# Optimization experiments

Hardware: AMD Instinct MI355X
Metric: run time of the kernel (lower is better)

Reference implementation:

```python
import jax, jax.numpy as jnp
import numpy as np

B, L, D1, D2, N = 4, 2048, 1024, 1024, 4096

def setup_inputs() -> dict:
    key = jax.random.key(0)
    k1, k2, k3 = jax.random.split(key, 3)
    inputs = jax.random.normal(k1, (B, L, D1), dtype=jnp.float32)
    key_param_tokens = jax.random.normal(k2, (N, D1), dtype=jnp.float32) * 0.02
    value_param_tokens = jax.random.normal(k3, (N, D2), dtype=jnp.float32) * 0.02
    return {"inputs": inputs, "key_param_tokens": key_param_tokens, "value_param_tokens": value_param_tokens}

def reference(inputs, key_param_tokens, value_param_tokens):
    # scores: [B, L, N] = query @ key^T (scale_factor = 1, no mask, dropout_p = 0)
    attn_weight = jnp.einsum('bld,nd->bln', inputs, key_param_tokens)
    n = attn_weight.shape[-1]
    # 'l2_norm_gelu': L2-normalize over the param-token axis, rescale by sqrt(n), then exact GELU
    l2 = jnp.sqrt(jnp.sum(attn_weight * attn_weight, axis=-1, keepdims=True))
    normed = attn_weight / l2 * jnp.sqrt(jnp.asarray(n, attn_weight.dtype))
    attn_weight = jax.nn.gelu(normed, approximate=False)
    # output: [B, L, D2]
    return jnp.einsum('bln,nd->bld', attn_weight, value_param_tokens)
```

## Files before the change

kernel.cpp:

```cpp
#include <hip/hip_runtime.h>
#include <hip/hip_bf16.h>
#include <math.h>
#include <stdint.h>

typedef __attribute__((ext_vector_type(8))) short short8;
typedef __attribute__((ext_vector_type(4))) float f32x4;

__device__ inline short f2bf(float x) {
  union { float f; uint32_t u; } c; c.f = x;
  uint32_t r = (c.u + 0x7FFFu + ((c.u >> 16) & 1u)) >> 16;
  return (short)(uint16_t)r;
}
__device__ inline float bf2f(short s) {
  union { uint32_t u; float f; } c; c.u = ((uint32_t)(uint16_t)s) << 16;
  return c.f;
}

__device__ inline void gload16(const short* src, const char* ldsdst) {
  __builtin_amdgcn_global_load_lds(
      (const __attribute__((address_space(1))) void*)src,
      (__attribute__((address_space(3))) void*)ldsdst, 16, 0, 0);
}

#define BAR __builtin_amdgcn_s_barrier()
#define VMC(n) asm volatile("s_waitcnt vmcnt(" #n ")" ::: "memory")

__global__ void f32_to_bf16_kernel(const float* __restrict__ in,
                                   short* __restrict__ out, int n8) {
  int i = blockIdx.x * blockDim.x + threadIdx.x;
  if (i >= n8) return;
  const float4* p = (const float4*)(in + (size_t)i * 8);
  float4 a = p[0], b = p[1];
  short8 o;
  o[0] = f2bf(a.x); o[1] = f2bf(a.y); o[2] = f2bf(a.z); o[3] = f2bf(a.w);
  o[4] = f2bf(b.x); o[5] = f2bf(b.y); o[6] = f2bf(b.z); o[7] = f2bf(b.w);
  *(short8*)(out + (size_t)i * 8) = o;
}

__global__ void transpose_bf16_kernel(const float* __restrict__ V,
                                      short* __restrict__ Vt,
                                      int rows, int cols) {
  __shared__ float tile[64][65];
  int n0 = blockIdx.x * 64;
  int d0 = blockIdx.y * 64;
  int t = threadIdx.x;
#pragma unroll
  for (int r = 0; r < 16; ++r) {
    int idx = t + 256 * r;
    int rr = idx >> 6, cc = idx & 63;
    tile[rr][cc] = V[(size_t)(n0 + rr) * cols + d0 + cc];
  }
  __syncthreads();
#pragma unroll
  for (int r = 0; r < 16; ++r) {
    int idx = t + 256 * r;
    int dd = idx >> 6, nn = idx & 63;
    Vt[(size_t)(d0 + dd) * rows + n0 + nn] = f2bf(tile[nn][dd]);
  }
}

__global__ __launch_bounds__(512, 2) void gemm1_kernel(
    const short* __restrict__ A, const short* __restrict__ B,
    short* __restrict__ S, float* __restrict__ rowss) {
  constexpr int K = 1024, N = 4096, NT = K / 64;
  __shared__ char lds[2 * 65536];
  const int t = threadIdx.x, lane = t & 63, w = t >> 6;
  const int wm = w >> 2, wn = w & 3;
  const int idx = lane & 15, g = lane >> 4;
  const int bid = blockIdx.x;
  const int id2 = (bid & 7) * 64 + (bid >> 3);
  const int row0 = (id2 >> 4) * 256, col0 = (id2 & 15) * 256;

  const int srow = t >> 3;
  const int ksl = (t & 7) ^ (srow & 7);
  const short* gA = A + (size_t)(row0 + srow) * K + ksl * 8;
  const short* gB = B + (size_t)(col0 + srow) * K + ksl * 8;

  auto stageA = [&](int buf, int frow, int kt) {
#pragma unroll
    for (int r = 0; r < 2; ++r)
      gload16(gA + (size_t)(frow + r * 64) * K + kt,
              &lds[buf * 65536 + (frow + r * 64) * 128 + t * 16]);
  };
  auto stageB = [&](int buf, int frow, int kt) {
#pragma unroll
    for (int r = 0; r < 2; ++r)
      gload16(gB + (size_t)(frow + r * 64) * K + kt,
              &lds[buf * 65536 + 32768 + (frow + r * 64) * 128 + t * 16]);
  };

  const int xv = (idx & 7) << 4;
  short8 a[4][2], b[2][2][2];
  auto lda = [&](int buf, int mh) {
#pragma unroll
    for (int f = 0; f < 4; ++f)
#pragma unroll
      for (int ks = 0; ks < 2; ++ks) {
        int row = mh * 128 + wm * 64 + f * 16 + idx;
        int byte = row * 128 + ((ks * 64 + g * 16) ^ xv);
        a[f][ks] = *(const short8*)&lds[buf * 65536 + byte];
      }
  };
  auto ldb = [&](int buf, int nh) {
#pragma unroll
    for (int nf = 0; nf < 2; ++nf)
#pragma unroll
      for (int ks = 0; ks < 2; ++ks) {
        int col = nh * 128 + wn * 32 + nf * 16 + idx;
        int byte = col * 128 + ((ks * 64 + g * 16) ^ xv);
        b[nh][nf][ks] = *(const short8*)&lds[buf * 65536 + 32768 + byte];
      }
  };

  f32x4 acc[8][4] = {};
  auto MF = [&](int mh, int nh) {
    __builtin_amdgcn_s_setprio(1);
#pragma unroll
    for (int ks = 0; ks < 2; ++ks)
#pragma unroll
      for (int f = 0; f < 4; ++f)
#pragma unroll
        for (int n = 0; n < 2; ++n)
          acc[mh * 4 + f][nh * 2 + n] = __builtin_amdgcn_mfma_f32_16x16x32_bf16(
              a[f][ks], b[nh][n][ks], acc[mh * 4 + f][nh * 2 + n], 0, 0, 0);
    __builtin_amdgcn_s_setprio(0);
  };

  stageA(0, 0, 0);
  stageB(0, 0, 0);
  stageB(0, 128, 0);
  stageA(0, 128, 0);
  VMC(2);
  BAR;

  for (int tb = 0; tb < NT; tb += 2) {
#pragma unroll
    for (int u = 0; u < 2; ++u) {
      const int T = tb + u, buf = u, nbuf = u ^ 1;
      const int kt1 = (T + 1) * 64;
      const bool more = (T + 1 < NT);
      lda(buf, 0); ldb(buf, 0);
      if (more) stageA(nbuf, 0, kt1);
      MF(0, 0);
      ldb(buf, 1);
      if (more) stageB(nbuf, 0, kt1);
      MF(0, 1);
      if (more) { VMC(4); } else { VMC(0); }
      BAR;
      lda(buf, 1);
      if (more) stageB(nbuf, 128, kt1);
      MF(1, 1);
      if (more) stageA(nbuf, 128, kt1);
      MF(1, 0);
      if (more) {
        VMC(2);
        BAR;
      }
    }
  }

#pragma unroll
  for (int mf = 0; mf < 8; ++mf) {
#pragma unroll
    for (int j = 0; j < 4; ++j) {
      const int row = row0 + wm * 64 + (mf & 3) * 16 + (mf >> 2) * 128 + g * 4 + j;
      float ss = 0.f;
#pragma unroll
      for (int nf = 0; nf < 4; ++nf) {
        const float v = acc[mf][nf][j];
        ss += v * v;
        const int col = col0 + wn * 32 + (nf & 1) * 16 + (nf >> 1) * 128 + idx;
        S[(size_t)row * N + col] = f2bf(v);
      }
      ss += __shfl_xor(ss, 1);
      ss += __shfl_xor(ss, 2);
      ss += __shfl_xor(ss, 4);
      ss += __shfl_xor(ss, 8);
      if (idx == 0) atomicAdd(&rowss[row], ss);
    }
  }
}

__global__ __launch_bounds__(512, 2) void gemm2_kernel(
    const short* __restrict__ A, const short* __restrict__ B,
    float* __restrict__ C) {
  constexpr int K = 4096, N = 1024, NT = K / 64;
  __shared__ char lds[2 * 49152];
  const int t = threadIdx.x, lane = t & 63, w = t >> 6;
  const int wm = w >> 1, wn = w & 1;
  const int idx = lane & 15, g = lane >> 4;
  const int bid = blockIdx.x;
  const int id2 = (bid & 7) * 32 + (bid >> 3);
  const int row0 = (id2 >> 3) * 256, col0 = (id2 & 7) * 128;

  const int srow = t >> 3;
  const int ksl = (t & 7) ^ (srow & 7);
  const short* gA = A + (size_t)(row0 + srow) * K + ksl * 8;
  const short* gB = B + (size_t)(col0 + srow) * K + ksl * 8;

  auto stageAr = [&](int buf, int fr, int kt) {
    gload16(gA + (size_t)(fr)*K + kt, &lds[buf * 49152 + fr * 128 + t * 16]);
  };
  auto stageB = [&](int buf, int kt) {
#pragma unroll
    for (int r = 0; r < 2; ++r)
      gload16(gB + (size_t)(r * 64) * K + kt,
              &lds[buf * 49152 + 32768 + r * 8192 + t * 16]);
  };

  const int xv = (idx & 7) << 4;
  short8 a[2][2], b[4][2];
  auto lda = [&](int buf, int mh) {
#pragma unroll
    for (int f = 0; f < 2; ++f)
#pragma unroll
      for (int ks = 0; ks < 2; ++ks) {
        int row = mh * 128 + wm * 32 + f * 16 + idx;
        int byte = row * 128 + ((ks * 64 + g * 16) ^ xv);
        a[f][ks] = *(const short8*)&lds[buf * 49152 + byte];
      }
  };
  auto ldb = [&](int buf) {
#pragma unroll
    for (int nf = 0; nf < 4; ++nf)
#pragma unroll
      for (int ks = 0; ks < 2; ++ks) {
        int col = wn * 64 + nf * 16 + idx;
        int byte = col * 128 + ((ks * 64 + g * 16) ^ xv);
        b[nf][ks] = *(const short8*)&lds[buf * 49152 + 32768 + byte];
      }
  };

  f32x4 acc[4][4] = {};
  auto MF = [&](int mh) {
    __builtin_amdgcn_s_setprio(1);
#pragma unroll
    for (int ks = 0; ks < 2; ++ks)
#pragma unroll
      for (int f = 0; f < 2; ++f)
#pragma unroll
        for (int nf = 0; nf < 4; ++nf)
          acc[mh * 2 + f][nf] = __builtin_amdgcn_mfma_f32_16x16x32_bf16(
              a[f][ks], b[nf][ks], acc[mh * 2 + f][nf], 0, 0, 0);
    __builtin_amdgcn_s_setprio(0);
  };

  stageB(0, 0);
  stageAr(0, 0, 0);
  stageAr(0, 64, 0);
  stageAr(0, 128, 0);
  stageAr(0, 192, 0);
  VMC(2);
  BAR;

  for (int tb = 0; tb < NT; tb += 2) {
#pragma unroll
    for (int u = 0; u < 2; ++u) {
      const int T = tb + u, buf = u, nbuf = u ^ 1;
      const int kt1 = (T + 1) * 64;
      const bool more = (T + 1 < NT);
      ldb(buf); lda(buf, 0);
      if (more) { stageB(nbuf, kt1); stageAr(nbuf, 0, kt1); stageAr(nbuf, 64, kt1); }
      MF(0);
      if (more) { VMC(4); } else { VMC(0); }
      BAR;
      lda(buf, 1);
      if (more) { stageAr(nbuf, 128, kt1); stageAr(nbuf, 192, kt1); }
      MF(1);
      if (more) {
        VMC(2);
        BAR;
      }
    }
  }

#pragma unroll
  for (int mf = 0; mf < 4; ++mf)
#pragma unroll
    for (int j = 0; j < 4; ++j) {
      const int row = row0 + wm * 32 + (mf & 1) * 16 + (mf >> 1) * 128 + g * 4 + j;
#pragma unroll
      for (int nf = 0; nf < 4; ++nf)
        C[(size_t)row * N + col0 + wn * 64 + nf * 16 + idx] = acc[mf][nf][j];
    }
}

__global__ void norm_gelu_kernel(short* __restrict__ S,
                                 const float* __restrict__ rowss, int total8) {
  int i = blockIdx.x * blockDim.x + threadIdx.x;
  if (i >= total8) return;
  size_t base = (size_t)i * 8;
  int row = (int)(base >> 12);
  float scale = 64.0f * rsqrtf(rowss[row]);
  short8 v = *(short8*)(S + base);
  short8 o;
#pragma unroll
  for (int k = 0; k < 8; ++k) {
    float x = bf2f(v[k]) * scale;
    float gl = 0.5f * x * (1.0f + erff(x * 0.70710678118654752f));
    o[k] = f2bf(gl);
  }
  *(short8*)(S + base) = o;
}

extern "C" void kernel_launch(void* const* d_in, const int* in_sizes, int n_in,
                              void* d_out, int out_size, void* d_ws,
                              size_t ws_size, hipStream_t stream) {
  const float* X = (const float*)d_in[0];
  const float* Kp = (const float*)d_in[1];
  const float* Vp = (const float*)d_in[2];
  float* out = (float*)d_out;

  const int M = 8192, D1 = 1024, Nn = 4096, D2 = 1024;

  char* ws = (char*)d_ws;
  short* Xb = (short*)ws; ws += (size_t)M * D1 * 2;
  short* Kb = (short*)ws; ws += (size_t)Nn * D1 * 2;
  short* Vt = (short*)ws; ws += (size_t)D2 * Nn * 2;
  short* S  = (short*)ws; ws += (size_t)M * Nn * 2;
  float* rowss = (float*)ws;
  (void)ws_size;

  hipMemsetAsync(rowss, 0, M * sizeof(float), stream);
  f32_to_bf16_kernel<<<(M * D1 / 8 + 255) / 256, 256, 0, stream>>>(X, Xb, M * D1 / 8);
  f32_to_bf16_kernel<<<(Nn * D1 / 8 + 255) / 256, 256, 0, stream>>>(Kp, Kb, Nn * D1 / 8);
  transpose_bf16_kernel<<<dim3(Nn / 64, D2 / 64), 256, 0, stream>>>(Vp, Vt, Nn, D2);

  gemm1_kernel<<<512, 512, 0, stream>>>(Xb, Kb, S, rowss);
  norm_gelu_kernel<<<(M * Nn / 8 + 255) / 256, 256, 0, stream>>>(S, rowss, M * Nn / 8);
  gemm2_kernel<<<256, 512, 0, stream>>>(S, Vt, out);
}
```

Baseline: 194.4 us.

## Switch both GEMMs to 32x32x16 MFMA tiles and merge conversion kernels

Both GEMM kernels now use the 32x32x16 bf16 MFMA instruction instead of 16x16x32. Fragment loads, LDS swizzle offsets, accumulator layout and epilogue row/column mapping are rewritten to match, including an extra shuffle in the row sum-of-squares reduction. The larger MFMA tile means fewer instructions and fewer LDS fragment reads per FLOP, at the cost of a different register layout and wider per-lane accumulators. The two fp32-to-bf16 conversion launches are also fused into a single kernel to save a launch.

```diff
diff --git a/kernel.cpp b/kernel.cpp
--- a/kernel.cpp
+++ b/kernel.cpp
@@ -4,7 +4,7 @@
 #include <stdint.h>
 
 typedef __attribute__((ext_vector_type(8))) short short8;
-typedef __attribute__((ext_vector_type(4))) float f32x4;
+typedef __attribute__((ext_vector_type(16))) float f32x16;
 
 __device__ inline short f2bf(float x) {
   union { float f; uint32_t u; } c; c.f = x;
@@ -25,16 +25,19 @@
 #define BAR __builtin_amdgcn_s_barrier()
 #define VMC(n) asm volatile("s_waitcnt vmcnt(" #n ")" ::: "memory")
 
-__global__ void f32_to_bf16_kernel(const float* __restrict__ in,
-                                   short* __restrict__ out, int n8) {
+__global__ void cvt2_kernel(const float* __restrict__ X, const float* __restrict__ Kp,
+                            short* __restrict__ Xb, short* __restrict__ Kb,
+                            int n8x, int n8tot) {
   int i = blockIdx.x * blockDim.x + threadIdx.x;
-  if (i >= n8) return;
-  const float4* p = (const float4*)(in + (size_t)i * 8);
+  if (i >= n8tot) return;
+  const float* src = (i < n8x) ? X + (size_t)i * 8 : Kp + (size_t)(i - n8x) * 8;
+  short* dst = (i < n8x) ? Xb + (size_t)i * 8 : Kb + (size_t)(i - n8x) * 8;
+  const float4* p = (const float4*)src;
   float4 a = p[0], b = p[1];
   short8 o;
   o[0] = f2bf(a.x); o[1] = f2bf(a.y); o[2] = f2bf(a.z); o[3] = f2bf(a.w);
   o[4] = f2bf(b.x); o[5] = f2bf(b.y); o[6] = f2bf(b.z); o[7] = f2bf(b.w);
-  *(short8*)(out + (size_t)i * 8) = o;
+  *(short8*)dst = o;
 }
 
 __global__ void transpose_bf16_kernel(const float* __restrict__ V,
@@ -66,15 +69,14 @@
   __shared__ char lds[2 * 65536];
   const int t = threadIdx.x, lane = t & 63, w = t >> 6;
   const int wm = w >> 2, wn = w & 3;
-  const int idx = lane & 15, g = lane >> 4;
+  const int r32 = lane & 31, l5 = lane >> 5;
   const int bid = blockIdx.x;
   const int id2 = (bid & 7) * 64 + (bid >> 3);
   const int row0 = (id2 >> 4) * 256, col0 = (id2 & 15) * 256;
 
-  const int srow = t >> 3;
-  const int ksl = (t & 7) ^ (srow & 7);
-  const short* gA = A + (size_t)(row0 + srow) * K + ksl * 8;
-  const short* gB = B + (size_t)(col0 + srow) * K + ksl * 8;
+  const int sxor = ((t & 7) ^ ((t >> 3) & 7)) * 8;
+  const short* gA = A + (size_t)(row0 + (t >> 3)) * K + sxor;
+  const short* gB = B + (size_t)(col0 + (t >> 3)) * K + sxor;
 
   auto stageA = [&](int buf, int frow, int kt) {
 #pragma unroll
@@ -89,40 +91,37 @@
               &lds[buf * 65536 + 32768 + (frow + r * 64) * 128 + t * 16]);
   };
 
-  const int xv = (idx & 7) << 4;
-  short8 a[4][2], b[2][2][2];
+  int qb[4];
+#pragma unroll
+  for (int c = 0; c < 4; ++c) qb[c] = ((c * 2 + l5) ^ (r32 & 7)) << 4;
+
+  short8 a[2][4], b[2][4];
   auto lda = [&](int buf, int mh) {
 #pragma unroll
-    for (int f = 0; f < 4; ++f)
-#pragma unroll
-      for (int ks = 0; ks < 2; ++ks) {
-        int row = mh * 128 + wm * 64 + f * 16 + idx;
-        int byte = row * 128 + ((ks * 64 + g * 16) ^ xv);
-        a[f][ks] = *(const short8*)&lds[buf * 65536 + byte];
+    for (int fr = 0; fr < 2; ++fr)
+#pragma unroll
+      for (int c = 0; c < 4; ++c) {
+        const int row = mh * 128 + wm * 64 + fr * 32 + r32;
+        a[fr][c] = *(const short8*)&lds[buf * 65536 + row * 128 + qb[c]];
       }
   };
   auto ldb = [&](int buf, int nh) {
 #pragma unroll
-    for (int nf = 0; nf < 2; ++nf)
-#pragma unroll
-      for (int ks = 0; ks < 2; ++ks) {
-        int col = nh * 128 + wn * 32 + nf * 16 + idx;
-        int byte = col * 128 + ((ks * 64 + g * 16) ^ xv);
-        b[nh][nf][ks] = *(const short8*)&lds[buf * 65536 + 32768 + byte];
-      }
-  };
-
-  f32x4 acc[8][4] = {};
-  auto MF = [&](int mh, int nh) {
+    for (int c = 0; c < 4; ++c) {
+      const int col = wn * 64 + nh * 32 + r32;
+      b[nh][c] = *(const short8*)&lds[buf * 65536 + 32768 + col * 128 + qb[c]];
+    }
+  };
+
+  f32x16 acc[4][2] = {};
+  auto MFQ = [&](int mh, int nh) {
     __builtin_amdgcn_s_setprio(1);
 #pragma unroll
-    for (int ks = 0; ks < 2; ++ks)
-#pragma unroll
-      for (int f = 0; f < 4; ++f)
-#pragma unroll
-        for (int n = 0; n < 2; ++n)
-          acc[mh * 4 + f][nh * 2 + n] = __builtin_amdgcn_mfma_f32_16x16x32_bf16(
-              a[f][ks], b[nh][n][ks], acc[mh * 4 + f][nh * 2 + n], 0, 0, 0);
+    for (int c = 0; c < 4; ++c)
+#pragma unroll
+      for (int fr = 0; fr < 2; ++fr)
+        acc[mh * 2 + fr][nh] = __builtin_amdgcn_mfma_f32_32x32x16_bf16(
+            a[fr][c], b[nh][c], acc[mh * 2 + fr][nh], 0, 0, 0);
     __builtin_amdgcn_s_setprio(0);
   };
 
@@ -141,17 +140,17 @@
       const bool more = (T + 1 < NT);
       lda(buf, 0); ldb(buf, 0);
       if (more) stageA(nbuf, 0, kt1);
-      MF(0, 0);
+      MFQ(0, 0);
       ldb(buf, 1);
       if (more) stageB(nbuf, 0, kt1);
-      MF(0, 1);
+      MFQ(0, 1);
       if (more) { VMC(4); } else { VMC(0); }
       BAR;
       lda(buf, 1);
       if (more) stageB(nbuf, 128, kt1);
-      MF(1, 1);
+      MFQ(1, 1);
       if (more) stageA(nbuf, 128, kt1);
-      MF(1, 0);
+      MFQ(1, 0);
       if (more) {
         VMC(2);
         BAR;
@@ -160,23 +159,25 @@
   }
 
 #pragma unroll
-  for (int mf = 0; mf < 8; ++mf) {
-#pragma unroll
-    for (int j = 0; j < 4; ++j) {
-      const int row = row0 + wm * 64 + (mf & 3) * 16 + (mf >> 2) * 128 + g * 4 + j;
+  for (int mf = 0; mf < 4; ++mf) {
+    const int mh = mf >> 1, fr = mf & 1;
+#pragma unroll
+    for (int j = 0; j < 16; ++j) {
+      const int row = row0 + mh * 128 + wm * 64 + fr * 32 +
+                      (j & 3) + 8 * (j >> 2) + 4 * l5;
       float ss = 0.f;
 #pragma unroll
-      for (int nf = 0; nf < 4; ++nf) {
-        const float v = acc[mf][nf][j];
+      for (int nh = 0; nh < 2; ++nh) {
+        const float v = acc[mf][nh][j];
         ss += v * v;
-        const int col = col0 + wn * 32 + (nf & 1) * 16 + (nf >> 1) * 128 + idx;
-        S[(size_t)row * N + col] = f2bf(v);
+        S[(size_t)row * N + col0 + wn * 64 + nh * 32 + r32] = f2bf(v);
       }
       ss += __shfl_xor(ss, 1);
       ss += __shfl_xor(ss, 2);
       ss += __shfl_xor(ss, 4);
       ss += __shfl_xor(ss, 8);
-      if (idx == 0) atomicAdd(&rowss[row], ss);
+      ss += __shfl_xor(ss, 16);
+      if (r32 == 0) atomicAdd(&rowss[row], ss);
     }
   }
 }
@@ -188,15 +189,14 @@
   __shared__ char lds[2 * 49152];
   const int t = threadIdx.x, lane = t & 63, w = t >> 6;
   const int wm = w >> 1, wn = w & 1;
-  const int idx = lane & 15, g = lane >> 4;
+  const int r32 = lane & 31, l5 = lane >> 5;
   const int bid = blockIdx.x;
   const int id2 = (bid & 7) * 32 + (bid >> 3);
   const int row0 = (id2 >> 3) * 256, col0 = (id2 & 7) * 128;
 
-  const int srow = t >> 3;
-  const int ksl = (t & 7) ^ (srow & 7);
-  const short* gA = A + (size_t)(row0 + srow) * K + ksl * 8;
-  const short* gB = B + (size_t)(col0 + srow) * K + ksl * 8;
+  const int sxor = ((t & 7) ^ ((t >> 3) & 7)) * 8;
+  const short* gA = A + (size_t)(row0 + (t >> 3)) * K + sxor;
+  const short* gB = B + (size_t)(col0 + (t >> 3)) * K + sxor;
 
   auto stageAr = [&](int buf, int fr, int kt) {
     gload16(gA + (size_t)(fr)*K + kt, &lds[buf * 49152 + fr * 128 + t * 16]);
@@ -208,40 +208,37 @@
               &lds[buf * 49152 + 32768 + r * 8192 + t * 16]);
   };
 
-  const int xv = (idx & 7) << 4;
-  short8 a[2][2], b[4][2];
+  int qb[4];
+#pragma unroll
+  for (int c = 0; c < 4; ++c) qb[c] = ((c * 2 + l5) ^ (r32 & 7)) << 4;
+
+  short8 a[4], b[2][4];
   auto lda = [&](int buf, int mh) {
 #pragma unroll
-    for (int f = 0; f < 2; ++f)
-#pragma unroll
-      for (int ks = 0; ks < 2; ++ks) {
-        int row = mh * 128 + wm * 32 + f * 16 + idx;
-        int byte = row * 128 + ((ks * 64 + g * 16) ^ xv);
-        a[f][ks] = *(const short8*)&lds[buf * 49152 + byte];
-      }
+    for (int c = 0; c < 4; ++c) {
+      const int row = mh * 128 + wm * 32 + r32;
+      a[c] = *(const short8*)&lds[buf * 49152 + row * 128 + qb[c]];
+    }
   };
   auto ldb = [&](int buf) {
 #pragma unroll
-    for (int nf = 0; nf < 4; ++nf)
-#pragma unroll
-      for (int ks = 0; ks < 2; ++ks) {
-        int col = wn * 64 + nf * 16 + idx;
-        int byte = col * 128 + ((ks * 64 + g * 16) ^ xv);
-        b[nf][ks] = *(const short8*)&lds[buf * 49152 + 32768 + byte];
-      }
-  };
-
-  f32x4 acc[4][4] = {};
+    for (int nf = 0; nf < 2; ++nf)
+#pragma unroll
+      for (int c = 0; c < 4; ++c) {
+        const int col = wn * 64 + nf * 32 + r32;
+        b[nf][c] = *(const short8*)&lds[buf * 49152 + 32768 + col * 128 + qb[c]];
+      }
+  };
+
+  f32x16 acc[2][2] = {};
   auto MF = [&](int mh) {
     __builtin_amdgcn_s_setprio(1);
 #pragma unroll
-    for (int ks = 0; ks < 2; ++ks)
-#pragma unroll
-      for (int f = 0; f < 2; ++f)
-#pragma unroll
-        for (int nf = 0; nf < 4; ++nf)
-          acc[mh * 2 + f][nf] = __builtin_amdgcn_mfma_f32_16x16x32_bf16(
-              a[f][ks], b[nf][ks], acc[mh * 2 + f][nf], 0, 0, 0);
+    for (int c = 0; c < 4; ++c)
+#pragma unroll
+      for (int nf = 0; nf < 2; ++nf)
+        acc[mh][nf] = __builtin_amdgcn_mfma_f32_32x32x16_bf16(
+            a[c], b[nf][c], acc[mh][nf], 0, 0, 0);
     __builtin_amdgcn_s_setprio(0);
   };
 
@@ -275,13 +272,13 @@
   }
 
 #pragma unroll
-  for (int mf = 0; mf < 4; ++mf)
-#pragma unroll
-    for (int j = 0; j < 4; ++j) {
-      const int row = row0 + wm * 32 + (mf & 1) * 16 + (mf >> 1) * 128 + g * 4 + j;
-#pragma unroll
-      for (int nf = 0; nf < 4; ++nf)
-        C[(size_t)row * N + col0 + wn * 64 + nf * 16 + idx] = acc[mf][nf][j];
+  for (int mh = 0; mh < 2; ++mh)
+#pragma unroll
+    for (int j = 0; j < 16; ++j) {
+      const int row = row0 + mh * 128 + wm * 32 + (j & 3) + 8 * (j >> 2) + 4 * l5;
+#pragma unroll
+      for (int nf = 0; nf < 2; ++nf)
+        C[(size_t)row * N + col0 + wn * 64 + nf * 32 + r32] = acc[mh][nf][j];
     }
 }
 
@@ -322,8 +319,8 @@
   (void)ws_size;
 
   hipMemsetAsync(rowss, 0, M * sizeof(float), stream);
-  f32_to_bf16_kernel<<<(M * D1 / 8 + 255) / 256, 256, 0, stream>>>(X, Xb, M * D1 / 8);
-  f32_to_bf16_kernel<<<(Nn * D1 / 8 + 255) / 256, 256, 0, stream>>>(Kp, Kb, Nn * D1 / 8);
+  const int n8x = M * D1 / 8, n8k = Nn * D1 / 8;
+  cvt2_kernel<<<(n8x + n8k + 255) / 256, 256, 0, stream>>>(X, Kp, Xb, Kb, n8x, n8x + n8k);
   transpose_bf16_kernel<<<dim3(Nn / 64, D2 / 64), 256, 0, stream>>>(Vp, Vt, Nn, D2);
 
   gemm1_kernel<<<512, 512, 0, stream>>>(Xb, Kb, S, rowss);
```

New measurement: 264.0 us. 1.36x slower.

## Restructure gemm1 into quadrant schedule with deeper B prefetch and merged conversions

Applied to the files above, without the earlier changes.

Reorganizes the gemm1 warp tiling so each wave owns a contiguous 128-row by 64-column quadrant. The main loop is rescheduled into four quadrant MFMA phases with barriers and explicit lgkmcnt waits, and B tiles are prefetched two k-steps ahead while A tiles are prefetched one step ahead. The two f32-to-bf16 conversion launches are also merged into a single kernel to save a launch. The extra barriers per phase may add synchronization stalls that offset the gain from deeper prefetch.

```diff
diff --git a/kernel.cpp b/kernel.cpp
--- a/kernel.cpp
+++ b/kernel.cpp
@@ -24,17 +24,25 @@
 
 #define BAR __builtin_amdgcn_s_barrier()
 #define VMC(n) asm volatile("s_waitcnt vmcnt(" #n ")" ::: "memory")
-
-__global__ void f32_to_bf16_kernel(const float* __restrict__ in,
-                                   short* __restrict__ out, int n8) {
+#define LGKM0                                          \
+  do {                                                 \
+    asm volatile("s_waitcnt lgkmcnt(0)" ::: "memory"); \
+    __builtin_amdgcn_sched_barrier(0);                 \
+  } while (0)
+
+__global__ void cvt2_kernel(const float* __restrict__ X, const float* __restrict__ Kp,
+                            short* __restrict__ Xb, short* __restrict__ Kb,
+                            int n8x, int n8tot) {
   int i = blockIdx.x * blockDim.x + threadIdx.x;
-  if (i >= n8) return;
-  const float4* p = (const float4*)(in + (size_t)i * 8);
+  if (i >= n8tot) return;
+  const float* src = (i < n8x) ? X + (size_t)i * 8 : Kp + (size_t)(i - n8x) * 8;
+  short* dst = (i < n8x) ? Xb + (size_t)i * 8 : Kb + (size_t)(i - n8x) * 8;
+  const float4* p = (const float4*)src;
   float4 a = p[0], b = p[1];
   short8 o;
   o[0] = f2bf(a.x); o[1] = f2bf(a.y); o[2] = f2bf(a.z); o[3] = f2bf(a.w);
   o[4] = f2bf(b.x); o[5] = f2bf(b.y); o[6] = f2bf(b.z); o[7] = f2bf(b.w);
-  *(short8*)(out + (size_t)i * 8) = o;
+  *(short8*)dst = o;
 }
 
 __global__ void transpose_bf16_kernel(const float* __restrict__ V,
@@ -71,90 +79,90 @@
   const int id2 = (bid & 7) * 64 + (bid >> 3);
   const int row0 = (id2 >> 4) * 256, col0 = (id2 & 15) * 256;
 
-  const int srow = t >> 3;
-  const int ksl = (t & 7) ^ (srow & 7);
-  const short* gA = A + (size_t)(row0 + srow) * K + ksl * 8;
-  const short* gB = B + (size_t)(col0 + srow) * K + ksl * 8;
-
-  auto stageA = [&](int buf, int frow, int kt) {
+  const int sxor = ((t & 7) ^ ((t >> 3) & 7)) * 8;
+  const short* gA = A + (size_t)(row0 + (t >> 3)) * K + sxor;
+  const short* gB = B + (size_t)(col0 + (t >> 3)) * K + sxor;
+
+  auto STGA = [&](int buf, int h, int T) {
 #pragma unroll
     for (int r = 0; r < 2; ++r)
-      gload16(gA + (size_t)(frow + r * 64) * K + kt,
-              &lds[buf * 65536 + (frow + r * 64) * 128 + t * 16]);
-  };
-  auto stageB = [&](int buf, int frow, int kt) {
+      gload16(gA + (size_t)(h * 128 + r * 64) * K + T * 64,
+              &lds[buf * 65536 + h * 16384 + r * 8192 + t * 16]);
+  };
+  auto STGB = [&](int buf, int h, int T) {
 #pragma unroll
     for (int r = 0; r < 2; ++r)
-      gload16(gB + (size_t)(frow + r * 64) * K + kt,
-              &lds[buf * 65536 + 32768 + (frow + r * 64) * 128 + t * 16]);
+      gload16(gB + (size_t)(h * 128 + r * 64) * K + T * 64,
+              &lds[buf * 65536 + 32768 + h * 16384 + r * 8192 + t * 16]);
   };
 
   const int xv = (idx & 7) << 4;
-  short8 a[4][2], b[2][2][2];
-  auto lda = [&](int buf, int mh) {
+  short8 a[4][2], b0[2][2], b1[2][2];
+  auto LDA = [&](int buf, int qm) {
 #pragma unroll
     for (int f = 0; f < 4; ++f)
 #pragma unroll
       for (int ks = 0; ks < 2; ++ks) {
-        int row = mh * 128 + wm * 64 + f * 16 + idx;
-        int byte = row * 128 + ((ks * 64 + g * 16) ^ xv);
-        a[f][ks] = *(const short8*)&lds[buf * 65536 + byte];
-      }
-  };
-  auto ldb = [&](int buf, int nh) {
-#pragma unroll
-    for (int nf = 0; nf < 2; ++nf)
+        const int rl = qm * 64 + f * 16 + idx;
+        a[f][ks] = *(const short8*)&lds[buf * 65536 + wm * 16384 + rl * 128 +
+                                        ((ks * 64 + g * 16) ^ xv)];
+      }
+  };
+  auto LDB = [&](int buf, int qn, short8(&bb)[2][2]) {
+#pragma unroll
+    for (int f = 0; f < 2; ++f)
 #pragma unroll
       for (int ks = 0; ks < 2; ++ks) {
-        int col = nh * 128 + wn * 32 + nf * 16 + idx;
-        int byte = col * 128 + ((ks * 64 + g * 16) ^ xv);
-        b[nh][nf][ks] = *(const short8*)&lds[buf * 65536 + 32768 + byte];
+        const int cl = (wn & 1) * 64 + qn * 32 + f * 16 + idx;
+        bb[f][ks] = *(const short8*)&lds[buf * 65536 + 32768 + (wn >> 1) * 16384 +
+                                         cl * 128 + ((ks * 64 + g * 16) ^ xv)];
       }
   };
 
   f32x4 acc[8][4] = {};
-  auto MF = [&](int mh, int nh) {
+  auto MFQ = [&](int qm, int qn, short8(&bb)[2][2]) {
     __builtin_amdgcn_s_setprio(1);
 #pragma unroll
     for (int ks = 0; ks < 2; ++ks)
 #pragma unroll
       for (int f = 0; f < 4; ++f)
 #pragma unroll
-        for (int n = 0; n < 2; ++n)
-          acc[mh * 4 + f][nh * 2 + n] = __builtin_amdgcn_mfma_f32_16x16x32_bf16(
-              a[f][ks], b[nh][n][ks], acc[mh * 4 + f][nh * 2 + n], 0, 0, 0);
+        for (int f2 = 0; f2 < 2; ++f2)
+          acc[qm * 4 + f][qn * 2 + f2] = __builtin_amdgcn_mfma_f32_16x16x32_bf16(
+              a[f][ks], bb[f2][ks], acc[qm * 4 + f][qn * 2 + f2], 0, 0, 0);
     __builtin_amdgcn_s_setprio(0);
   };
 
-  stageA(0, 0, 0);
-  stageB(0, 0, 0);
-  stageB(0, 128, 0);
-  stageA(0, 128, 0);
-  VMC(2);
+  STGA(0, 0, 0); STGA(0, 1, 0);
+  STGB(0, 0, 0); STGB(0, 1, 0);
+  STGB(1, 0, 1); STGB(1, 1, 1);
+  VMC(4);
   BAR;
 
   for (int tb = 0; tb < NT; tb += 2) {
 #pragma unroll
     for (int u = 0; u < 2; ++u) {
       const int T = tb + u, buf = u, nbuf = u ^ 1;
-      const int kt1 = (T + 1) * 64;
-      const bool more = (T + 1 < NT);
-      lda(buf, 0); ldb(buf, 0);
-      if (more) stageA(nbuf, 0, kt1);
-      MF(0, 0);
-      ldb(buf, 1);
-      if (more) stageB(nbuf, 0, kt1);
-      MF(0, 1);
-      if (more) { VMC(4); } else { VMC(0); }
+      const bool more1 = (T + 1 < NT), more2 = (T + 2 < NT);
+      LDA(buf, 0);
+      LDB(buf, 0, b0);
+      if (more1) STGA(nbuf, 0, T + 1);
+      BAR; LGKM0; MFQ(0, 0, b0); BAR;
+      LDB(buf, 1, b1);
+      if (more1) STGA(nbuf, 1, T + 1);
+      BAR; LGKM0; MFQ(0, 1, b1); BAR;
+      LDA(buf, 1);
+      if (more2) STGB(buf, 0, T + 2);
+      BAR; LGKM0; MFQ(1, 1, b1); BAR;
+      if (more2) STGB(buf, 1, T + 2);
       BAR;
-      lda(buf, 1);
-      if (more) stageB(nbuf, 128, kt1);
-      MF(1, 1);
-      if (more) stageA(nbuf, 128, kt1);
-      MF(1, 0);
-      if (more) {
-        VMC(2);
+      MFQ(1, 0, b0);
+      if (more2) {
+        VMC(4);
         BAR;
+      } else if (more1) {
+        VMC(0);
+        BAR;
       }
     }
   }
@@ -163,13 +171,13 @@
   for (int mf = 0; mf < 8; ++mf) {
 #pragma unroll
     for (int j = 0; j < 4; ++j) {
-      const int row = row0 + wm * 64 + (mf & 3) * 16 + (mf >> 2) * 128 + g * 4 + j;
+      const int row = row0 + wm * 128 + (mf >> 2) * 64 + (mf & 3) * 16 + g * 4 + j;
       float ss = 0.f;
 #pragma unroll
       for (int nf = 0; nf < 4; ++nf) {
         const float v = acc[mf][nf][j];
         ss += v * v;
-        const int col = col0 + wn * 32 + (nf & 1) * 16 + (nf >> 1) * 128 + idx;
+        const int col = col0 + wn * 64 + (nf >> 1) * 32 + (nf & 1) * 16 + idx;
         S[(size_t)row * N + col] = f2bf(v);
       }
       ss += __shfl_xor(ss, 1);
@@ -322,8 +330,8 @@
   (void)ws_size;
 
   hipMemsetAsync(rowss, 0, M * sizeof(float), stream);
-  f32_to_bf16_kernel<<<(M * D1 / 8 + 255) / 256, 256, 0, stream>>>(X, Xb, M * D1 / 8);
-  f32_to_bf16_kernel<<<(Nn * D1 / 8 + 255) / 256, 256, 0, stream>>>(Kp, Kb, Nn * D1 / 8);
+  const int n8x = M * D1 / 8, n8k = Nn * D1 / 8;
+  cvt2_kernel<<<(n8x + n8k + 255) / 256, 256, 0, stream>>>(X, Kp, Xb, Kb, n8x, n8x + n8k);
   transpose_bf16_kernel<<<dim3(Nn / 64, D2 / 64), 256, 0, stream>>>(Vp, Vt, Nn, D2);
 
   gemm1_kernel<<<512, 512, 0, stream>>>(Xb, Kb, S, rowss);
```

Result: no change. 198.1 us (+1.9%).

## Restructure gemm2 pipeline around N-halves and merge input conversion kernels

Applied to the files above, without the earlier changes.

Gemm2 now has each wave hold all four A fragments and split the work across two N-halves of B fragments instead of two M-halves. Staging is reordered: the whole A tile for the next step loads at once, and the B tile is prefetched two steps ahead, with explicit lgkmcnt waits and extra barriers. Separately, the two fp32-to-bf16 conversion launches for X and K are merged into one kernel to save a launch. The extra barriers and the changed prefetch distance could help or hurt overlap between loads and MFMA work.

```diff
diff --git a/kernel.cpp b/kernel.cpp
--- a/kernel.cpp
+++ b/kernel.cpp
@@ -24,17 +24,21 @@
 
 #define BAR __builtin_amdgcn_s_barrier()
 #define VMC(n) asm volatile("s_waitcnt vmcnt(" #n ")" ::: "memory")
-
-__global__ void f32_to_bf16_kernel(const float* __restrict__ in,
-                                   short* __restrict__ out, int n8) {
+#define LGKMW asm volatile("s_waitcnt lgkmcnt(0)" ::: "memory")
+
+__global__ void cvt2_kernel(const float* __restrict__ X, const float* __restrict__ Kp,
+                            short* __restrict__ Xb, short* __restrict__ Kb,
+                            int n8x, int n8tot) {
   int i = blockIdx.x * blockDim.x + threadIdx.x;
-  if (i >= n8) return;
-  const float4* p = (const float4*)(in + (size_t)i * 8);
+  if (i >= n8tot) return;
+  const float* src = (i < n8x) ? X + (size_t)i * 8 : Kp + (size_t)(i - n8x) * 8;
+  short* dst = (i < n8x) ? Xb + (size_t)i * 8 : Kb + (size_t)(i - n8x) * 8;
+  const float4* p = (const float4*)src;
   float4 a = p[0], b = p[1];
   short8 o;
   o[0] = f2bf(a.x); o[1] = f2bf(a.y); o[2] = f2bf(a.z); o[3] = f2bf(a.w);
   o[4] = f2bf(b.x); o[5] = f2bf(b.y); o[6] = f2bf(b.z); o[7] = f2bf(b.w);
-  *(short8*)(out + (size_t)i * 8) = o;
+  *(short8*)dst = o;
 }
 
 __global__ void transpose_bf16_kernel(const float* __restrict__ V,
@@ -198,58 +202,59 @@
   const short* gA = A + (size_t)(row0 + srow) * K + ksl * 8;
   const short* gB = B + (size_t)(col0 + srow) * K + ksl * 8;
 
-  auto stageAr = [&](int buf, int fr, int kt) {
-    gload16(gA + (size_t)(fr)*K + kt, &lds[buf * 49152 + fr * 128 + t * 16]);
-  };
-  auto stageB = [&](int buf, int kt) {
+  auto STGA = [&](int buf, int T) {
+#pragma unroll
+    for (int r = 0; r < 4; ++r)
+      gload16(gA + (size_t)(r * 64) * K + T * 64,
+              &lds[buf * 49152 + r * 8192 + t * 16]);
+  };
+  auto STGB = [&](int buf, int T) {
 #pragma unroll
     for (int r = 0; r < 2; ++r)
-      gload16(gB + (size_t)(r * 64) * K + kt,
+      gload16(gB + (size_t)(r * 64) * K + T * 64,
               &lds[buf * 49152 + 32768 + r * 8192 + t * 16]);
   };
 
   const int xv = (idx & 7) << 4;
-  short8 a[2][2], b[4][2];
-  auto lda = [&](int buf, int mh) {
+  short8 a[4][2], b[2][2];
+  auto LDA = [&](int buf) {
+#pragma unroll
+    for (int f = 0; f < 4; ++f)
+#pragma unroll
+      for (int ks = 0; ks < 2; ++ks) {
+        int row = wm * 64 + f * 16 + idx;
+        a[f][ks] = *(const short8*)&lds[buf * 49152 + row * 128 +
+                                        ((ks * 64 + g * 16) ^ xv)];
+      }
+  };
+  auto LDB = [&](int buf, int nh) {
 #pragma unroll
     for (int f = 0; f < 2; ++f)
 #pragma unroll
       for (int ks = 0; ks < 2; ++ks) {
-        int row = mh * 128 + wm * 32 + f * 16 + idx;
-        int byte = row * 128 + ((ks * 64 + g * 16) ^ xv);
-        a[f][ks] = *(const short8*)&lds[buf * 49152 + byte];
-      }
-  };
-  auto ldb = [&](int buf) {
-#pragma unroll
-    for (int nf = 0; nf < 4; ++nf)
-#pragma unroll
-      for (int ks = 0; ks < 2; ++ks) {
-        int col = wn * 64 + nf * 16 + idx;
-        int byte = col * 128 + ((ks * 64 + g * 16) ^ xv);
-        b[nf][ks] = *(const short8*)&lds[buf * 49152 + 32768 + byte];
+        int col = wn * 64 + nh * 32 + f * 16 + idx;
+        b[f][ks] = *(const short8*)&lds[buf * 49152 + 32768 + col * 128 +
+                                        ((ks * 64 + g * 16) ^ xv)];
       }
   };
 
   f32x4 acc[4][4] = {};
-  auto MF = [&](int mh) {
+  auto MFQ = [&](int nh) {
     __builtin_amdgcn_s_setprio(1);
 #pragma unroll
     for (int ks = 0; ks < 2; ++ks)
 #pragma unroll
-      for (int f = 0; f < 2; ++f)
-#pragma unroll
-        for (int nf = 0; nf < 4; ++nf)
-          acc[mh * 2 + f][nf] = __builtin_amdgcn_mfma_f32_16x16x32_bf16(
-              a[f][ks], b[nf][ks], acc[mh * 2 + f][nf], 0, 0, 0);
+      for (int f = 0; f < 4; ++f)
+#pragma unroll
+        for (int f2 = 0; f2 < 2; ++f2)
+          acc[f][nh * 2 + f2] = __builtin_amdgcn_mfma_f32_16x16x32_bf16(
+              a[f][ks], b[f2][ks], acc[f][nh * 2 + f2], 0, 0, 0);
     __builtin_amdgcn_s_setprio(0);
   };
 
-  stageB(0, 0);
-  stageAr(0, 0, 0);
-  stageAr(0, 64, 0);
-  stageAr(0, 128, 0);
-  stageAr(0, 192, 0);
+  STGA(0, 0);
+  STGB(0, 0);
+  STGB(1, 1);
   VMC(2);
   BAR;
 
@@ -257,20 +262,21 @@
 #pragma unroll
     for (int u = 0; u < 2; ++u) {
       const int T = tb + u, buf = u, nbuf = u ^ 1;
-      const int kt1 = (T + 1) * 64;
-      const bool more = (T + 1 < NT);
-      ldb(buf); lda(buf, 0);
-      if (more) { stageB(nbuf, kt1); stageAr(nbuf, 0, kt1); stageAr(nbuf, 64, kt1); }
-      MF(0);
-      if (more) { VMC(4); } else { VMC(0); }
-      BAR;
-      lda(buf, 1);
-      if (more) { stageAr(nbuf, 128, kt1); stageAr(nbuf, 192, kt1); }
-      MF(1);
-      if (more) {
-        VMC(2);
-        BAR;
-      }
+      const bool more1 = (T + 1 < NT), more2 = (T + 2 < NT);
+      LDA(buf);
+      LDB(buf, 0);
+      if (more1) STGA(nbuf, T + 1);
+      BAR;
+      LGKMW;
+      MFQ(0);
+      BAR;
+      LDB(buf, 1);
+      BAR;
+      LGKMW;
+      if (more2) STGB(buf, T + 2);
+      MFQ(1);
+      if (more2) { VMC(2); } else if (more1) { VMC(0); }
+      BAR;
     }
   }
 
@@ -278,7 +284,7 @@
   for (int mf = 0; mf < 4; ++mf)
 #pragma unroll
     for (int j = 0; j < 4; ++j) {
-      const int row = row0 + wm * 32 + (mf & 1) * 16 + (mf >> 1) * 128 + g * 4 + j;
+      const int row = row0 + wm * 64 + mf * 16 + g * 4 + j;
 #pragma unroll
       for (int nf = 0; nf < 4; ++nf)
         C[(size_t)row * N + col0 + wn * 64 + nf * 16 + idx] = acc[mf][nf][j];
@@ -322,8 +328,8 @@
   (void)ws_size;
 
   hipMemsetAsync(rowss, 0, M * sizeof(float), stream);
-  f32_to_bf16_kernel<<<(M * D1 / 8 + 255) / 256, 256, 0, stream>>>(X, Xb, M * D1 / 8);
-  f32_to_bf16_kernel<<<(Nn * D1 / 8 + 255) / 256, 256, 0, stream>>>(Kp, Kb, Nn * D1 / 8);
+  const int n8x = M * D1 / 8, n8k = Nn * D1 / 8;
+  cvt2_kernel<<<(n8x + n8k + 255) / 256, 256, 0, stream>>>(X, Kp, Xb, Kb, n8x, n8x + n8k);
   transpose_bf16_kernel<<<dim3(Nn / 64, D2 / 64), 256, 0, stream>>>(Vp, Vt, Nn, D2);
 
   gemm1_kernel<<<512, 512, 0, stream>>>(Xb, Kb, S, rowss);
```

Measured after the change: 195.2 us. About the same (+0.4%).
